# Performance work log

Measured on AMD Instinct MI355X. Metric: run time of the kernel, lower is better.

Reference implementation:

```python
import jax, jax.numpy as jnp
import numpy as np

EMBED = 1024
HEADS = 16
HEAD_DIM = EMBED // HEADS


def setup_inputs() -> dict:
    key = jax.random.key(0)
    ks = jax.random.split(key, 6)
    N, S = 2, 2048
    scale = 1.0 / np.sqrt(EMBED)
    x = jax.random.normal(ks[0], (N, S, EMBED), dtype=jnp.float32)
    # nn.Linear weights are [out, in]; y = x @ W.T
    Wq = jax.random.normal(ks[1], (EMBED, EMBED), dtype=jnp.float32) * scale
    Wk = jax.random.normal(ks[2], (EMBED, EMBED), dtype=jnp.float32) * scale
    Wv = jax.random.normal(ks[3], (EMBED, EMBED), dtype=jnp.float32) * scale
    Wo = jax.random.normal(ks[4], (EMBED, EMBED), dtype=jnp.float32) * scale
    bo = jax.random.normal(ks[5], (EMBED,), dtype=jnp.float32) * 0.01
    return {"x": x, "Wq": Wq, "Wk": Wk, "Wv": Wv, "Wo": Wo, "bo": bo}


def reference(x, Wq, Wk, Wv, Wo, bo):
    N, S, E = x.shape
    # projections (torch Linear: x @ W.T)
    def split_heads(t):
        return t.reshape(N, S, HEADS, HEAD_DIM).transpose(0, 2, 1, 3)  # [N,H,S,D]
    q = split_heads(x @ Wq.T)
    k = split_heads(x @ Wk.T)
    v = split_heads(x @ Wv.T)
    # scores scaled by sqrt(embed_size), faithful to original
    scores = jnp.einsum('nhqd,nhkd->nhqk', q, k) / jnp.sqrt(jnp.float32(E))
    attn = jax.nn.softmax(scores, axis=-1)
    out = jnp.einsum('nhqk,nhkd->nhqd', attn, v)  # [N,H,S,D]
    out = out.transpose(0, 2, 1, 3).reshape(N, S, E)
    return out @ Wo.T + bo
```

## Files before the change

kernel.cpp:

```cpp
#include <hip/hip_runtime.h>

#define E   1024
#define SQ  2048
#define NR  4096

typedef _Float16 half8  __attribute__((ext_vector_type(8)));
typedef _Float16 half4  __attribute__((ext_vector_type(4)));
typedef __fp16   fp16x2 __attribute__((ext_vector_type(2)));
typedef float    f32x4  __attribute__((ext_vector_type(4)));

#define MFMA_F16(a, b, c) __builtin_amdgcn_mfma_f32_16x16x32_f16((a), (b), (c), 0, 0, 0)

#if __has_builtin(__builtin_amdgcn_exp2f)
#define EXP2(x) __builtin_amdgcn_exp2f(x)
#else
#define EXP2(x) exp2f(x)
#endif

#define QSCALE 0.04508422002778011f

__device__ __forceinline__ void async16(const void* g, void* l) {
  __builtin_amdgcn_global_load_lds((const __attribute__((address_space(1))) void*)g,
                                   (__attribute__((address_space(3))) void*)l, 16, 0, 0);
}

__device__ __forceinline__ float bperm_f(int srclane, float v) {
  return __int_as_float(__builtin_amdgcn_ds_bpermute(srclane << 2, __float_as_int(v)));
}

__global__ __launch_bounds__(256)
void cvtall(const float* __restrict__ x, const float* __restrict__ wq,
            const float* __restrict__ wk, const float* __restrict__ wv,
            const float* __restrict__ wo,
            _Float16* __restrict__ xh, _Float16* __restrict__ wqh,
            _Float16* __restrict__ wkh, _Float16* __restrict__ wvh,
            _Float16* __restrict__ woh) {
  int b = blockIdx.x;
  const float* src; _Float16* dst; int off;
  if (b < 4096)      { src = x;  dst = xh;  off = b; }
  else if (b < 5120) { src = wq; dst = wqh; off = b - 4096; }
  else if (b < 6144) { src = wk; dst = wkh; off = b - 5120; }
  else if (b < 7168) { src = wv; dst = wvh; off = b - 6144; }
  else               { src = wo; dst = woh; off = b - 7168; }
  int i = off * 256 + threadIdx.x;
  f32x4 v = ((const f32x4*)src)[i];
  ((half4*)dst)[i] = __builtin_convertvector(v, half4);
}

__global__ __launch_bounds__(256, 2)
void gemm_qkv(const _Float16* __restrict__ A,
              const _Float16* __restrict__ B0, const _Float16* __restrict__ B1,
              const _Float16* __restrict__ B2,
              _Float16* __restrict__ C0, _Float16* __restrict__ C1,
              _Float16* __restrict__ Vg2,
              int M, int N, int K)
{
  const int z = blockIdx.z;
  const _Float16* B = (z == 0) ? B0 : ((z == 1) ? B1 : B2);
  __shared__ _Float16 As[128 * 64];
  __shared__ _Float16 Bs[128 * 64];
  const int tid = threadIdx.x;
  const int w = tid >> 6, lane = tid & 63;
  const int lr = lane & 15, lg = lane >> 4;
  const int l8 = lane >> 3, l7 = lane & 7;
  const int gch = l7 ^ (l8 & 7);
  const int tm = blockIdx.x * 128, tn = blockIdx.y * 128;
  const int wr = w >> 1, wc = w & 1;
  const int sl7 = lr & 7;

  const f32x4 zv = {0.f, 0.f, 0.f, 0.f};
  f32x4 acc[4][4];
  #pragma unroll
  for (int mi = 0; mi < 4; mi++)
    #pragma unroll
    for (int ni = 0; ni < 4; ni++) acc[mi][ni] = zv;

  for (int ks = 0; ks < K; ks += 64) {
    #pragma unroll
    for (int ci = 0; ci < 4; ci++) {
      int c = w + ci * 4;
      async16(A + (size_t)(tm + c * 8 + l8) * K + ks + gch * 8, (void*)(As + c * 512));
    }
    #pragma unroll
    for (int ci = 0; ci < 4; ci++) {
      int c = w + ci * 4;
      async16(B + (size_t)(tn + c * 8 + l8) * K + ks + gch * 8, (void*)(Bs + c * 512));
    }
    __syncthreads();
    #pragma unroll
    for (int kk = 0; kk < 2; kk++) {
      const int sl = ((kk * 4 + lg) ^ sl7) << 4;
      half8 af[4], bf[4];
      #pragma unroll
      for (int mi = 0; mi < 4; mi++)
        af[mi] = *(const half8*)((const char*)As + (wr * 64 + mi * 16 + lr) * 128 + sl);
      #pragma unroll
      for (int ni = 0; ni < 4; ni++)
        bf[ni] = *(const half8*)((const char*)Bs + (wc * 64 + ni * 16 + lr) * 128 + sl);
      #pragma unroll
      for (int mi = 0; mi < 4; mi++)
        #pragma unroll
        for (int ni = 0; ni < 4; ni++)
          acc[mi][ni] = MFMA_F16(af[mi], bf[ni], acc[mi][ni]);
    }
    __syncthreads();
  }
  if (z == 2) {
    #pragma unroll
    for (int mi = 0; mi < 4; mi++) {
      const int row = tm + wr * 64 + mi * 16 + 4 * lg;
      const int n = row >> 11;
      const int s0 = (row & 2047) & ~63;
      const int cb = 32 * (mi >> 1) + 8 * lg + 4 * (mi & 1);
      #pragma unroll
      for (int ni = 0; ni < 4; ni++) {
        const int d = tn + wc * 64 + ni * 16 + lr;
        const int nb = n * 16 + (d >> 6);
        half4 hv = __builtin_convertvector(acc[mi][ni], half4);
        *(half4*)(Vg2 + ((size_t)nb * 64 + (d & 63)) * SQ + s0 + cb) = hv;
      }
    }
  } else {
    _Float16* C = (z == 0) ? C0 : C1;
    const float sc = (z == 0) ? QSCALE : 1.0f;
    #pragma unroll
    for (int mi = 0; mi < 4; mi++) {
      const int row = tm + wr * 64 + mi * 16 + 4 * lg;
      #pragma unroll
      for (int ni = 0; ni < 4; ni++) {
        const int col = tn + wc * 64 + ni * 16 + lr;
        #pragma unroll
        for (int j = 0; j < 4; j++)
          C[(size_t)(row + j) * N + col] = (_Float16)(acc[mi][ni][j] * sc);
      }
    }
  }
}

__global__ __launch_bounds__(256, 2)
void gemm_o(const _Float16* __restrict__ A, const _Float16* __restrict__ B,
            float* __restrict__ Cf, const float* __restrict__ bias,
            int M, int N, int K)
{
  __shared__ _Float16 As[64 * 64];
  __shared__ _Float16 Bs[128 * 64];
  const int tid = threadIdx.x;
  const int w = tid >> 6, lane = tid & 63;
  const int lr = lane & 15, lg = lane >> 4;
  const int l8 = lane >> 3, l7 = lane & 7;
  const int gch = l7 ^ (l8 & 7);
  const int tm = blockIdx.x * 64, tn = blockIdx.y * 128;
  const int wr = w >> 1, wc = w & 1;
  const int sl7 = lr & 7;

  const f32x4 zv = {0.f, 0.f, 0.f, 0.f};
  f32x4 acc[2][4];
  #pragma unroll
  for (int mi = 0; mi < 2; mi++)
    #pragma unroll
    for (int ni = 0; ni < 4; ni++) acc[mi][ni] = zv;

  for (int ks = 0; ks < K; ks += 64) {
    #pragma unroll
    for (int ci = 0; ci < 2; ci++) {
      int c = w + ci * 4;
      async16(A + (size_t)(tm + c * 8 + l8) * K + ks + gch * 8, (void*)(As + c * 512));
    }
    #pragma unroll
    for (int ci = 0; ci < 4; ci++) {
      int c = w + ci * 4;
      async16(B + (size_t)(tn + c * 8 + l8) * K + ks + gch * 8, (void*)(Bs + c * 512));
    }
    __syncthreads();
    #pragma unroll
    for (int kk = 0; kk < 2; kk++) {
      const int sl = ((kk * 4 + lg) ^ sl7) << 4;
      half8 af[2], bf[4];
      #pragma unroll
      for (int mi = 0; mi < 2; mi++)
        af[mi] = *(const half8*)((const char*)As + (wr * 32 + mi * 16 + lr) * 128 + sl);
      #pragma unroll
      for (int ni = 0; ni < 4; ni++)
        bf[ni] = *(const half8*)((const char*)Bs + (wc * 64 + ni * 16 + lr) * 128 + sl);
      #pragma unroll
      for (int mi = 0; mi < 2; mi++)
        #pragma unroll
        for (int ni = 0; ni < 4; ni++)
          acc[mi][ni] = MFMA_F16(af[mi], bf[ni], acc[mi][ni]);
    }
    __syncthreads();
  }
  #pragma unroll
  for (int mi = 0; mi < 2; mi++) {
    const int row = tm + wr * 32 + mi * 16 + 4 * lg;
    #pragma unroll
    for (int ni = 0; ni < 4; ni++) {
      const int col = tn + wc * 64 + ni * 16 + lr;
      #pragma unroll
      for (int j = 0; j < 4; j++)
        Cf[(size_t)(row + j) * N + col] = acc[mi][ni][j] + bias[col];
    }
  }
}

__global__ __launch_bounds__(256, 4)
void attn_kernel(const _Float16* __restrict__ Q, const _Float16* __restrict__ Kg,
                 const _Float16* __restrict__ Vg2, _Float16* __restrict__ Og)
{
  __shared__ _Float16 Ks[2][64 * 64];
  __shared__ _Float16 Vt[2][64 * 64];
  const int tid = threadIdx.x;
  const int w = tid >> 6, lane = tid & 63;
  const int lr = lane & 15, lg = lane >> 4;
  const int l8 = lane >> 3, l7 = lane & 7;
  const int id = blockIdx.x + 32 * blockIdx.y;
  const int wid = (id & 7) * 128 + (id >> 3);
  const int qb = wid & 31, nb = wid >> 5;
  const size_t hb  = (size_t)(nb >> 4) * SQ * E + (size_t)(nb & 15) * 64;
  const size_t hb2 = (size_t)nb * 64 * SQ;
  const int qbase = qb * 64 + w * 16;
  const int gsl = (l7 ^ (l8 & 7)) * 8;
  const int sl7 = lr & 7;

  half8 qf[2];
  #pragma unroll
  for (int kd = 0; kd < 2; kd++)
    qf[kd] = *(const half8*)(Q + hb + (size_t)(qbase + lr) * E + kd * 32 + lg * 8);

  const f32x4 zv = {0.f, 0.f, 0.f, 0.f};
  f32x4 o[4];
  float ms = -1e30f, ls = 0.f;
  #pragma unroll
  for (int nd = 0; nd < 4; nd++) o[nd] = zv;

  #pragma unroll
  for (int ci = 0; ci < 2; ci++) {
    int c = w + ci * 4;
    async16(Kg  + hb  + (size_t)(c * 8 + l8) * E  + gsl, (void*)(Ks[0] + c * 512));
    async16(Vg2 + hb2 + (size_t)(c * 8 + l8) * SQ + gsl, (void*)(Vt[0] + c * 512));
  }
  __syncthreads();

  int cur = 0;
  for (int t = 0; t < 32; t++) {
    if (t < 31) {
      const int kvb = (t + 1) * 64;
      #pragma unroll
      for (int ci = 0; ci < 2; ci++) {
        int c = w + ci * 4;
        async16(Kg  + hb  + (size_t)(kvb + c * 8 + l8) * E + gsl, (void*)(Ks[cur ^ 1] + c * 512));
        async16(Vg2 + hb2 + (size_t)(c * 8 + l8) * SQ + kvb + gsl, (void*)(Vt[cur ^ 1] + c * 512));
      }
    }
    f32x4 s[4];
    #pragma unroll
    for (int ni = 0; ni < 4; ni++) s[ni] = zv;
    #pragma unroll
    for (int kd = 0; kd < 2; kd++) {
      const int sl = ((kd * 4 + lg) ^ sl7) << 4;
      half8 kf[4];
      #pragma unroll
      for (int ni = 0; ni < 4; ni++)
        kf[ni] = *(const half8*)((const char*)Ks[cur] + (ni * 16 + lr) * 128 + sl);
      #pragma unroll
      for (int ni = 0; ni < 4; ni++)
        s[ni] = MFMA_F16(kf[ni], qf[kd], s[ni]);
    }
    {
      float m0 = fmaxf(fmaxf(s[0][0], s[0][1]), fmaxf(s[0][2], s[0][3]));
      float m1 = fmaxf(fmaxf(s[1][0], s[1][1]), fmaxf(s[1][2], s[1][3]));
      float m2 = fmaxf(fmaxf(s[2][0], s[2][1]), fmaxf(s[2][2], s[2][3]));
      float m3 = fmaxf(fmaxf(s[3][0], s[3][1]), fmaxf(s[3][2], s[3][3]));
      float mx = fmaxf(fmaxf(m0, m1), fmaxf(m2, m3));
      mx = fmaxf(mx, __shfl_xor(mx, 16));
      mx = fmaxf(mx, __shfl_xor(mx, 32));
      if (__all(mx <= ms + 8.0f)) {
        float rs = 0.f;
        #pragma unroll
        for (int ni = 0; ni < 4; ni++)
          #pragma unroll
          for (int jr = 0; jr < 4; jr++) {
            float p = EXP2(s[ni][jr] - ms);
            s[ni][jr] = p; rs += p;
          }
        rs += __shfl_xor(rs, 16);
        rs += __shfl_xor(rs, 32);
        ls += rs;
      } else {
        float mnew = fmaxf(ms, mx);
        float corr = EXP2(ms - mnew);
        ms = mnew;
        float rs = 0.f;
        #pragma unroll
        for (int ni = 0; ni < 4; ni++)
          #pragma unroll
          for (int jr = 0; jr < 4; jr++) {
            float p = EXP2(s[ni][jr] - ms);
            s[ni][jr] = p; rs += p;
          }
        rs += __shfl_xor(rs, 16);
        rs += __shfl_xor(rs, 32);
        ls = ls * corr + rs;
        #pragma unroll
        for (int jr = 0; jr < 4; jr++) {
          float c4 = bperm_f(4 * lg + jr, corr);
          #pragma unroll
          for (int nd = 0; nd < 4; nd++) o[nd][jr] *= c4;
        }
      }
    }
    half8 pa[2];
    #pragma unroll
    for (int kk = 0; kk < 2; kk++) {
      union { half8 h8; fp16x2 h2[4]; } u;
      u.h2[0] = __builtin_amdgcn_cvt_pkrtz(s[2 * kk][0], s[2 * kk][1]);
      u.h2[1] = __builtin_amdgcn_cvt_pkrtz(s[2 * kk][2], s[2 * kk][3]);
      u.h2[2] = __builtin_amdgcn_cvt_pkrtz(s[2 * kk + 1][0], s[2 * kk + 1][1]);
      u.h2[3] = __builtin_amdgcn_cvt_pkrtz(s[2 * kk + 1][2], s[2 * kk + 1][3]);
      pa[kk] = u.h8;
    }
    #pragma unroll
    for (int kk = 0; kk < 2; kk++) {
      const int sl = ((kk * 4 + lg) ^ sl7) << 4;
      half8 vf[4];
      #pragma unroll
      for (int nd = 0; nd < 4; nd++)
        vf[nd] = *(const half8*)((const char*)Vt[cur] + (nd * 16 + lr) * 128 + sl);
      #pragma unroll
      for (int nd = 0; nd < 4; nd++)
        o[nd] = MFMA_F16(pa[kk], vf[nd], o[nd]);
    }
    __syncthreads();
    cur ^= 1;
  }
  {
    float li = 1.0f / ls;
    #pragma unroll
    for (int jr = 0; jr < 4; jr++) {
      float lv = bperm_f(4 * lg + jr, li);
      const int row = qbase + 4 * lg + jr;
      #pragma unroll
      for (int nd = 0; nd < 4; nd++)
        Og[hb + (size_t)row * E + nd * 16 + lr] = (_Float16)(o[nd][jr] * lv);
    }
  }
}

extern "C" void kernel_launch(void* const* d_in, const int* in_sizes, int n_in,
                              void* d_out, int out_size, void* d_ws, size_t ws_size,
                              hipStream_t stream)
{
  const float* x  = (const float*)d_in[0];
  const float* Wq = (const float*)d_in[1];
  const float* Wk = (const float*)d_in[2];
  const float* Wv = (const float*)d_in[3];
  const float* Wo = (const float*)d_in[4];
  const float* bo = (const float*)d_in[5];
  char* ws = (char*)d_ws;
  const size_t MB = 1024u * 1024u;
  _Float16* xh  = (_Float16*)(ws);
  _Float16* Wqh = (_Float16*)(ws + 8 * MB);
  _Float16* Wkh = (_Float16*)(ws + 10 * MB);
  _Float16* Wvh = (_Float16*)(ws + 12 * MB);
  _Float16* Woh = (_Float16*)(ws + 14 * MB);
  _Float16* Vg2 = (_Float16*)(ws + 16 * MB);
  _Float16* Oh  = (_Float16*)(ws + 24 * MB);
  _Float16* Qh  = (_Float16*)(d_out);
  _Float16* Kh  = (_Float16*)((char*)d_out + 8 * MB);
  float* Y = (float*)d_out;

  cvtall<<<8192, 256, 0, stream>>>(x, Wq, Wk, Wv, Wo, xh, Wqh, Wkh, Wvh, Woh);

  gemm_qkv<<<dim3(32, 8, 3), 256, 0, stream>>>(
      xh, Wqh, Wkh, Wvh, Qh, Kh, Vg2, NR, E, E);

  attn_kernel<<<dim3(32, 32), 256, 0, stream>>>(Qh, Kh, Vg2, Oh);

  gemm_o<<<dim3(64, 8), 256, 0, stream>>>(Oh, Woh, Y, bo, NR, E, E);
}
```

Before: 186.7 us.

## Double-buffer LDS tiles in projection GEMMs and raise MFMA wave priority in attention

The QKV and output-projection GEMMs now use two LDS buffers, prefetching the next K-slice with async global-to-LDS loads while MFMAs run on the current one. This removes the load-then-wait stall at each iteration. The attention kernel wraps its two MFMA phases in s_setprio so matrix work is favored over the other waves on the CU, and the address math is hoisted into base pointers. The cost is doubled LDS per block: gemm_qkv reaches 64KB, which may lower occupancy, and gemm_o's launch bound is raised to 3 blocks.

Result: slower. 197.7 us (+5.9%).

```diff
diff --git a/kernel.cpp b/kernel.cpp
--- a/kernel.cpp
+++ b/kernel.cpp
@@ -57,8 +57,8 @@
 {
   const int z = blockIdx.z;
   const _Float16* B = (z == 0) ? B0 : ((z == 1) ? B1 : B2);
-  __shared__ _Float16 As[128 * 64];
-  __shared__ _Float16 Bs[128 * 64];
+  __shared__ _Float16 As[2][128 * 64];
+  __shared__ _Float16 Bs[2][128 * 64];
   const int tid = threadIdx.x;
   const int w = tid >> 6, lane = tid & 63;
   const int lr = lane & 15, lg = lane >> 4;
@@ -68,6 +68,9 @@
   const int wr = w >> 1, wc = w & 1;
   const int sl7 = lr & 7;
 
+  const _Float16* Ab = A + (size_t)(tm + w * 8 + l8) * K + gch * 8;
+  const _Float16* Bb = B + (size_t)(tn + w * 8 + l8) * K + gch * 8;
+
   const f32x4 zv = {0.f, 0.f, 0.f, 0.f};
   f32x4 acc[4][4];
   #pragma unroll
@@ -75,28 +78,34 @@
     #pragma unroll
     for (int ni = 0; ni < 4; ni++) acc[mi][ni] = zv;
 
+  #pragma unroll
+  for (int ci = 0; ci < 4; ci++) {
+    async16(Ab + (size_t)(ci * 32) * K, (void*)(As[0] + (w + ci * 4) * 512));
+    async16(Bb + (size_t)(ci * 32) * K, (void*)(Bs[0] + (w + ci * 4) * 512));
+  }
+  __syncthreads();
+
+  int cur = 0;
   for (int ks = 0; ks < K; ks += 64) {
-    #pragma unroll
-    for (int ci = 0; ci < 4; ci++) {
-      int c = w + ci * 4;
-      async16(A + (size_t)(tm + c * 8 + l8) * K + ks + gch * 8, (void*)(As + c * 512));
-    }
-    #pragma unroll
-    for (int ci = 0; ci < 4; ci++) {
-      int c = w + ci * 4;
-      async16(B + (size_t)(tn + c * 8 + l8) * K + ks + gch * 8, (void*)(Bs + c * 512));
-    }
-    __syncthreads();
+    if (ks + 64 < K) {
+      const _Float16* An = Ab + ks + 64;
+      const _Float16* Bn = Bb + ks + 64;
+      #pragma unroll
+      for (int ci = 0; ci < 4; ci++) {
+        async16(An + (size_t)(ci * 32) * K, (void*)(As[cur ^ 1] + (w + ci * 4) * 512));
+        async16(Bn + (size_t)(ci * 32) * K, (void*)(Bs[cur ^ 1] + (w + ci * 4) * 512));
+      }
+    }
     #pragma unroll
     for (int kk = 0; kk < 2; kk++) {
       const int sl = ((kk * 4 + lg) ^ sl7) << 4;
       half8 af[4], bf[4];
       #pragma unroll
       for (int mi = 0; mi < 4; mi++)
-        af[mi] = *(const half8*)((const char*)As + (wr * 64 + mi * 16 + lr) * 128 + sl);
+        af[mi] = *(const half8*)((const char*)As[cur] + (wr * 64 + mi * 16 + lr) * 128 + sl);
       #pragma unroll
       for (int ni = 0; ni < 4; ni++)
-        bf[ni] = *(const half8*)((const char*)Bs + (wc * 64 + ni * 16 + lr) * 128 + sl);
+        bf[ni] = *(const half8*)((const char*)Bs[cur] + (wc * 64 + ni * 16 + lr) * 128 + sl);
       #pragma unroll
       for (int mi = 0; mi < 4; mi++)
         #pragma unroll
@@ -104,6 +113,7 @@
           acc[mi][ni] = MFMA_F16(af[mi], bf[ni], acc[mi][ni]);
     }
     __syncthreads();
+    cur ^= 1;
   }
   if (z == 2) {
     #pragma unroll
@@ -137,13 +147,13 @@
   }
 }
 
-__global__ __launch_bounds__(256, 2)
+__global__ __launch_bounds__(256, 3)
 void gemm_o(const _Float16* __restrict__ A, const _Float16* __restrict__ B,
             float* __restrict__ Cf, const float* __restrict__ bias,
             int M, int N, int K)
 {
-  __shared__ _Float16 As[64 * 64];
-  __shared__ _Float16 Bs[128 * 64];
+  __shared__ _Float16 As[2][64 * 64];
+  __shared__ _Float16 Bs[2][128 * 64];
   const int tid = threadIdx.x;
   const int w = tid >> 6, lane = tid & 63;
   const int lr = lane & 15, lg = lane >> 4;
@@ -153,6 +163,9 @@
   const int wr = w >> 1, wc = w & 1;
   const int sl7 = lr & 7;
 
+  const _Float16* Ab = A + (size_t)(tm + w * 8 + l8) * K + gch * 8;
+  const _Float16* Bb = B + (size_t)(tn + w * 8 + l8) * K + gch * 8;
+
   const f32x4 zv = {0.f, 0.f, 0.f, 0.f};
   f32x4 acc[2][4];
   #pragma unroll
@@ -160,28 +173,36 @@
     #pragma unroll
     for (int ni = 0; ni < 4; ni++) acc[mi][ni] = zv;
 
+  #pragma unroll
+  for (int ci = 0; ci < 2; ci++)
+    async16(Ab + (size_t)(ci * 32) * K, (void*)(As[0] + (w + ci * 4) * 512));
+  #pragma unroll
+  for (int ci = 0; ci < 4; ci++)
+    async16(Bb + (size_t)(ci * 32) * K, (void*)(Bs[0] + (w + ci * 4) * 512));
+  __syncthreads();
+
+  int cur = 0;
   for (int ks = 0; ks < K; ks += 64) {
-    #pragma unroll
-    for (int ci = 0; ci < 2; ci++) {
-      int c = w + ci * 4;
-      async16(A + (size_t)(tm + c * 8 + l8) * K + ks + gch * 8, (void*)(As + c * 512));
-    }
-    #pragma unroll
-    for (int ci = 0; ci < 4; ci++) {
-      int c = w + ci * 4;
-      async16(B + (size_t)(tn + c * 8 + l8) * K + ks + gch * 8, (void*)(Bs + c * 512));
-    }
-    __syncthreads();
+    if (ks + 64 < K) {
+      const _Float16* An = Ab + ks + 64;
+      const _Float16* Bn = Bb + ks + 64;
+      #pragma unroll
+      for (int ci = 0; ci < 2; ci++)
+        async16(An + (size_t)(ci * 32) * K, (void*)(As[cur ^ 1] + (w + ci * 4) * 512));
+      #pragma unroll
+      for (int ci = 0; ci < 4; ci++)
+        async16(Bn + (size_t)(ci * 32) * K, (void*)(Bs[cur ^ 1] + (w + ci * 4) * 512));
+    }
     #pragma unroll
     for (int kk = 0; kk < 2; kk++) {
       const int sl = ((kk * 4 + lg) ^ sl7) << 4;
       half8 af[2], bf[4];
       #pragma unroll
       for (int mi = 0; mi < 2; mi++)
-        af[mi] = *(const half8*)((const char*)As + (wr * 32 + mi * 16 + lr) * 128 + sl);
+        af[mi] = *(const half8*)((const char*)As[cur] + (wr * 32 + mi * 16 + lr) * 128 + sl);
       #pragma unroll
       for (int ni = 0; ni < 4; ni++)
-        bf[ni] = *(const half8*)((const char*)Bs + (wc * 64 + ni * 16 + lr) * 128 + sl);
+        bf[ni] = *(const half8*)((const char*)Bs[cur] + (wc * 64 + ni * 16 + lr) * 128 + sl);
       #pragma unroll
       for (int mi = 0; mi < 2; mi++)
         #pragma unroll
@@ -189,6 +210,7 @@
           acc[mi][ni] = MFMA_F16(af[mi], bf[ni], acc[mi][ni]);
     }
     __syncthreads();
+    cur ^= 1;
   }
   #pragma unroll
   for (int mi = 0; mi < 2; mi++) {
@@ -222,6 +244,9 @@
   const int gsl = (l7 ^ (l8 & 7)) * 8;
   const int sl7 = lr & 7;
 
+  const _Float16* Kb = Kg  + hb  + (size_t)(w * 8 + l8) * E  + gsl;
+  const _Float16* Vb = Vg2 + hb2 + (size_t)(w * 8 + l8) * SQ + gsl;
+
   half8 qf[2];
   #pragma unroll
   for (int kd = 0; kd < 2; kd++)
@@ -235,9 +260,8 @@
 
   #pragma unroll
   for (int ci = 0; ci < 2; ci++) {
-    int c = w + ci * 4;
-    async16(Kg  + hb  + (size_t)(c * 8 + l8) * E  + gsl, (void*)(Ks[0] + c * 512));
-    async16(Vg2 + hb2 + (size_t)(c * 8 + l8) * SQ + gsl, (void*)(Vt[0] + c * 512));
+    async16(Kb + (size_t)(ci * 32) * E,  (void*)(Ks[0] + (w + ci * 4) * 512));
+    async16(Vb + (size_t)(ci * 32) * SQ, (void*)(Vt[0] + (w + ci * 4) * 512));
   }
   __syncthreads();
 
@@ -247,14 +271,14 @@
       const int kvb = (t + 1) * 64;
       #pragma unroll
       for (int ci = 0; ci < 2; ci++) {
-        int c = w + ci * 4;
-        async16(Kg  + hb  + (size_t)(kvb + c * 8 + l8) * E + gsl, (void*)(Ks[cur ^ 1] + c * 512));
-        async16(Vg2 + hb2 + (size_t)(c * 8 + l8) * SQ + kvb + gsl, (void*)(Vt[cur ^ 1] + c * 512));
+        async16(Kb + (size_t)(kvb + ci * 32) * E,  (void*)(Ks[cur ^ 1] + (w + ci * 4) * 512));
+        async16(Vb + (size_t)(ci * 32) * SQ + kvb, (void*)(Vt[cur ^ 1] + (w + ci * 4) * 512));
       }
     }
     f32x4 s[4];
     #pragma unroll
     for (int ni = 0; ni < 4; ni++) s[ni] = zv;
+    __builtin_amdgcn_s_setprio(1);
     #pragma unroll
     for (int kd = 0; kd < 2; kd++) {
       const int sl = ((kd * 4 + lg) ^ sl7) << 4;
@@ -266,6 +290,7 @@
       for (int ni = 0; ni < 4; ni++)
         s[ni] = MFMA_F16(kf[ni], qf[kd], s[ni]);
     }
+    __builtin_amdgcn_s_setprio(0);
     {
       float m0 = fmaxf(fmaxf(s[0][0], s[0][1]), fmaxf(s[0][2], s[0][3]));
       float m1 = fmaxf(fmaxf(s[1][0], s[1][1]), fmaxf(s[1][2], s[1][3]));
@@ -319,6 +344,7 @@
       u.h2[3] = __builtin_amdgcn_cvt_pkrtz(s[2 * kk + 1][2], s[2 * kk + 1][3]);
       pa[kk] = u.h8;
     }
+    __builtin_amdgcn_s_setprio(1);
     #pragma unroll
     for (int kk = 0; kk < 2; kk++) {
       const int sl = ((kk * 4 + lg) ^ sl7) << 4;
@@ -330,6 +356,7 @@
       for (int nd = 0; nd < 4; nd++)
         o[nd] = MFMA_F16(pa[kk], vf[nd], o[nd]);
     }
+    __builtin_amdgcn_s_setprio(0);
     __syncthreads();
     cur ^= 1;
   }
```
